# Kernel optimization log

Measured on AMD Instinct MI355X. Metric: run time of the kernel, lower is better.

The kernel has to match this reference:

```python
import jax, jax.numpy as jnp
import numpy as np

B, L, C = 1, 4096, 1024
H = 16
D = C // H  # head_dim = 64


def setup_inputs() -> dict:
    key = jax.random.key(0)
    k1, k2, k3 = jax.random.split(key, 3)
    scale_in = 1.0 / np.sqrt(C)
    return {
        "x": jax.random.normal(k1, (B, L, C), dtype=jnp.float32),
        "Wqkv": jax.random.normal(k2, (C, 3 * C), dtype=jnp.float32) * scale_in,
        "bqkv": jnp.zeros((3 * C,), dtype=jnp.float32),
        "Wout": jax.random.normal(k3, (C, C), dtype=jnp.float32) * scale_in,
        "bout": jnp.zeros((C,), dtype=jnp.float32),
    }


def reference(x, Wqkv, bqkv, Wout, bout):
    Bx, Lx, Cx = x.shape
    qkv = x @ Wqkv + bqkv                             # [B, L, 3C]
    qkv = qkv.reshape(Bx, Lx, 3, H, D)
    qkv = jnp.transpose(qkv, (2, 0, 3, 1, 4))         # [3, B, H, L, D]
    q, k, v = qkv[0], qkv[1], qkv[2]
    scores = jnp.einsum("bhqd,bhkd->bhqk", q, k) / jnp.sqrt(jnp.float32(D))
    # causal mask: strictly upper triangle -> -inf
    causal = jnp.triu(jnp.ones((Lx, Lx), dtype=bool), k=1)
    scores = jnp.where(causal, -jnp.inf, scores)
    attn = jax.nn.softmax(scores, axis=-1)            # [B, H, L, L]
    out = jnp.einsum("bhqk,bhkd->bhqd", attn, v)      # [B, H, L, D]
    out = jnp.transpose(out, (0, 2, 1, 3)).reshape(Bx, Lx, Cx)
    return out @ Wout + bout
```

## Files before the change

kernel.cpp:

```cpp
#include <hip/hip_runtime.h>
#include <hip/hip_bf16.h>

typedef unsigned short u16;
typedef __bf16 bf16x8 __attribute__((ext_vector_type(8)));
typedef float f32x4 __attribute__((ext_vector_type(4)));

#define L_SEQ 4096
#define CDIM  1024
#define NH    16
#define HD    64
#define N_QKV 3072
#define ATT_STRIDE 88

static __device__ __forceinline__ float bf2f(u16 u) {
    union { float f; unsigned int i; } v; v.i = ((unsigned int)u) << 16; return v.f;
}
static __device__ __forceinline__ u16 f2bf(float f) {
    union { float f; unsigned int i; } v; v.f = f;
    unsigned int u = v.i;
    return (u16)((u + 0x7fffu + ((u >> 16) & 1u)) >> 16);
}

static __device__ __forceinline__ f32x4 mfma16x16x32(bf16x8 a, bf16x8 b, f32x4 c) {
    return __builtin_amdgcn_mfma_f32_16x16x32_bf16(a, b, c, 0, 0, 0);
}

typedef const __attribute__((address_space(1))) unsigned int* gas_u32;
typedef __attribute__((address_space(3))) unsigned int* las_u32;
static __device__ __forceinline__ void gload_lds16(const u16* g, u16* l) {
    __builtin_amdgcn_global_load_lds((gas_u32)g, (las_u32)l, 16, 0, 0);
}

__global__ __launch_bounds__(256) void k_cast_x(const float* __restrict__ src,
                                                u16* __restrict__ dst, int n8) {
    int i = blockIdx.x * 256 + threadIdx.x;
    if (i >= n8) return;
    const float4* s = (const float4*)(src + (size_t)i * 8);
    float4 a = s[0], b = s[1];
    u16 o[8] = { f2bf(a.x), f2bf(a.y), f2bf(a.z), f2bf(a.w),
                 f2bf(b.x), f2bf(b.y), f2bf(b.z), f2bf(b.w) };
    *(uint4*)(dst + (size_t)i * 8) = *(uint4*)o;
}

__global__ __launch_bounds__(256) void k_transpose_cast(const float* __restrict__ src,
                                                        u16* __restrict__ dst,
                                                        int R, int C) {
    __shared__ u16 tile[32][33];
    int c0 = blockIdx.x * 32, r0 = blockIdx.y * 32;
    int tx = threadIdx.x & 31, ty = threadIdx.x >> 5;
#pragma unroll
    for (int i = 0; i < 32; i += 8)
        tile[ty + i][tx] = f2bf(src[(size_t)(r0 + ty + i) * C + c0 + tx]);
    __syncthreads();
#pragma unroll
    for (int i = 0; i < 32; i += 8)
        dst[(size_t)(c0 + ty + i) * R + r0 + tx] = tile[tx][ty + i];
}

__global__ __launch_bounds__(256) void k_transpose_v(const u16* __restrict__ qkv,
                                                     u16* __restrict__ vt) {
    __shared__ u16 tile[32][33];
    int k0 = blockIdx.x * 32, d0 = blockIdx.y * 32, h = blockIdx.z;
    int tx = threadIdx.x & 31, ty = threadIdx.x >> 5;
#pragma unroll
    for (int i = 0; i < 32; i += 8)
        tile[ty + i][tx] = qkv[(size_t)(k0 + ty + i) * N_QKV + 2 * CDIM + h * HD + d0 + tx];
    __syncthreads();
#pragma unroll
    for (int i = 0; i < 32; i += 8)
        vt[(size_t)(h * HD + d0 + ty + i) * L_SEQ + k0 + tx] = tile[tx][ty + i];
}

template <typename OutT>
__global__ __launch_bounds__(256) void k_gemm_bt(const u16* __restrict__ A,
                                                 const u16* __restrict__ Bt,
                                                 const float* __restrict__ bias,
                                                 OutT* __restrict__ Cmat,
                                                 int M, int N, int K) {
    __shared__ alignas(16) u16 As[128 * 32];
    __shared__ alignas(16) u16 Bs[128 * 32];
    int t = threadIdx.x;
    int n0 = blockIdx.x * 128, m0 = blockIdx.y * 128;
    int l = t & 63, w = t >> 6;
    int wm = (w >> 1) * 64, wn = (w & 1) * 64;
    int lr = l & 15, lq = l >> 4;

    const f32x4 vzero = {0.f, 0.f, 0.f, 0.f};
    f32x4 acc[4][4];
#pragma unroll
    for (int mi = 0; mi < 4; mi++)
#pragma unroll
        for (int ni = 0; ni < 4; ni++) acc[mi][ni] = vzero;

    int ar = t >> 2;
    int ac = (t & 3) * 8;
    const u16* Ag = A + (size_t)(m0 + ar) * K + ac;
    const u16* Bg = Bt + (size_t)(n0 + ar) * K + ac;
    u16* AsD0 = &As[t * 8];
    u16* AsD1 = &As[t * 8 + 64 * 32];
    u16* BsD0 = &Bs[t * 8];
    u16* BsD1 = &Bs[t * 8 + 64 * 32];

    for (int k0 = 0; k0 < K; k0 += 32) {
        gload_lds16(Ag + k0,                     AsD0);
        gload_lds16(Ag + (size_t)64 * K + k0,    AsD1);
        gload_lds16(Bg + k0,                     BsD0);
        gload_lds16(Bg + (size_t)64 * K + k0,    BsD1);
        __syncthreads();

        bf16x8 af[4], bfr[4];
#pragma unroll
        for (int mi = 0; mi < 4; mi++)
            af[mi] = *(const bf16x8*)&As[(wm + mi * 16 + lr) * 32 + lq * 8];
#pragma unroll
        for (int ni = 0; ni < 4; ni++)
            bfr[ni] = *(const bf16x8*)&Bs[(wn + ni * 16 + lr) * 32 + lq * 8];
#pragma unroll
        for (int mi = 0; mi < 4; mi++)
#pragma unroll
            for (int ni = 0; ni < 4; ni++)
                acc[mi][ni] = mfma16x16x32(af[mi], bfr[ni], acc[mi][ni]);
        __syncthreads();
    }

#pragma unroll
    for (int ni = 0; ni < 4; ni++) {
        int col = n0 + wn + ni * 16 + lr;
        float bv = bias[col];
#pragma unroll
        for (int mi = 0; mi < 4; mi++) {
            int row = m0 + wm + mi * 16 + lq * 4;
#pragma unroll
            for (int r = 0; r < 4; r++) {
                float v = acc[mi][ni][r] + bv;
                if constexpr (sizeof(OutT) == 2)
                    Cmat[(size_t)(row + r) * N + col] = f2bf(v);
                else
                    Cmat[(size_t)(row + r) * N + col] = v;
            }
        }
    }
}

__global__ __launch_bounds__(256) void k_attn(const u16* __restrict__ qkv,
                                              const u16* __restrict__ vt,
                                              u16* __restrict__ attn) {
    __shared__ alignas(16) u16 Ks[64 * ATT_STRIDE];
    __shared__ alignas(16) u16 Vs[64 * ATT_STRIDE];

    int t = threadIdx.x;
    int l = t & 63, w = t >> 6;
    int h = blockIdx.y;
    int lr = l & 15, lq = l >> 4;
    int row8 = t >> 3;
    int ch = (t & 7) * 8;
    int qloc = w * 16 + lr;

    const f32x4 vzero = {0.f, 0.f, 0.f, 0.f};
    const u16* Kbase = qkv + (size_t)row8 * N_QKV + CDIM + h * HD + ch;
    const u16* Vbase = vt + (size_t)(h * HD + row8) * L_SEQ + ch;

#pragma unroll
    for (int phase = 0; phase < 2; phase++) {
        int tile = phase ? (63 - blockIdx.x) : blockIdx.x;
        int q0 = tile * 64;
        int nkv = tile + 1;

        bf16x8 bq[2];
        {
            const u16* Qg = qkv + (size_t)(q0 + qloc) * N_QKV + h * HD + lq * 8;
            union { uint4 u; u16 hh[8]; } q0u, q1u;
            q0u.u = *(const uint4*)(Qg);
            q1u.u = *(const uint4*)(Qg + 32);
            union { bf16x8 v; u16 hh[8]; } f0, f1;
#pragma unroll
            for (int j = 0; j < 8; j++) {
                f0.hh[j] = f2bf(bf2f(q0u.hh[j]) * 0.125f);
                f1.hh[j] = f2bf(bf2f(q1u.hh[j]) * 0.125f);
            }
            bq[0] = f0.v; bq[1] = f1.v;
        }

        f32x4 o[4];
#pragma unroll
        for (int dt = 0; dt < 4; dt++) o[dt] = vzero;
        float m_i = -1e30f, l_i = 0.f;

        uint4 rk0, rk1, rv0, rv1;
        {
            const u16* Kg = Kbase;
            rk0 = *(const uint4*)Kg;
            rk1 = *(const uint4*)(Kg + (size_t)32 * N_QKV);
            const u16* Vg = Vbase;
            rv0 = *(const uint4*)Vg;
            rv1 = *(const uint4*)(Vg + (size_t)32 * L_SEQ);
        }

        for (int it = 0; it < nkv; ++it) {
            *(uint4*)&Ks[row8 * ATT_STRIDE + ch]        = rk0;
            *(uint4*)&Ks[(row8 + 32) * ATT_STRIDE + ch] = rk1;
            *(uint4*)&Vs[row8 * ATT_STRIDE + ch]        = rv0;
            *(uint4*)&Vs[(row8 + 32) * ATT_STRIDE + ch] = rv1;
            __syncthreads();

            if (it + 1 < nkv) {
                int k1 = (it + 1) * 64;
                const u16* Kg = Kbase + (size_t)k1 * N_QKV;
                rk0 = *(const uint4*)Kg;
                rk1 = *(const uint4*)(Kg + (size_t)32 * N_QKV);
                const u16* Vg = Vbase + k1;
                rv0 = *(const uint4*)Vg;
                rv1 = *(const uint4*)(Vg + (size_t)32 * L_SEQ);
            }

            f32x4 s[4];
#pragma unroll
            for (int nt = 0; nt < 4; nt++) s[nt] = vzero;
#pragma unroll
            for (int ks = 0; ks < 2; ks++)
#pragma unroll
                for (int nt = 0; nt < 4; nt++) {
                    bf16x8 ak = *(const bf16x8*)&Ks[(nt * 16 + lr) * ATT_STRIDE + ks * 32 + lq * 8];
                    s[nt] = mfma16x16x32(ak, bq[ks], s[nt]);
                }

            bool diag = ((it * 64) == q0);
            float tmax = -1e30f;
#pragma unroll
            for (int nt = 0; nt < 4; nt++)
#pragma unroll
                for (int r = 0; r < 4; r++) {
                    float v = s[nt][r];
                    if (diag && (nt * 16 + lq * 4 + r > qloc)) v = -1e30f;
                    s[nt][r] = v;
                    tmax = fmaxf(tmax, v);
                }
            tmax = fmaxf(tmax, __shfl_xor(tmax, 16));
            tmax = fmaxf(tmax, __shfl_xor(tmax, 32));

            float mnew = fmaxf(m_i, tmax);
            float alpha = __expf(m_i - mnew);
            float rsum = 0.f;
#pragma unroll
            for (int nt = 0; nt < 4; nt++)
#pragma unroll
                for (int r = 0; r < 4; r++) {
                    float e = __expf(s[nt][r] - mnew);
                    s[nt][r] = e;
                    rsum += e;
                }
            rsum += __shfl_xor(rsum, 16);
            rsum += __shfl_xor(rsum, 32);
            l_i = l_i * alpha + rsum;
            m_i = mnew;
#pragma unroll
            for (int dt = 0; dt < 4; dt++)
#pragma unroll
                for (int r = 0; r < 4; r++) o[dt][r] *= alpha;

#pragma unroll
            for (int a = 0; a < 2; a++) {
                union { bf16x8 v; u16 hh[8]; } bp;
#pragma unroll
                for (int r = 0; r < 4; r++) {
                    bp.hh[r]     = f2bf(s[2 * a][r]);
                    bp.hh[r + 4] = f2bf(s[2 * a + 1][r]);
                }
#pragma unroll
                for (int dt = 0; dt < 4; dt++) {
                    union { bf16x8 v; uint2 u2[2]; } av;
                    const u16* vrow = &Vs[(dt * 16 + lr) * ATT_STRIDE + a * 32 + lq * 4];
                    av.u2[0] = *(const uint2*)(vrow);
                    av.u2[1] = *(const uint2*)(vrow + 16);
                    o[dt] = mfma16x16x32(av.v, bp.v, o[dt]);
                }
            }
            __syncthreads();
        }

        float inv = 1.0f / l_i;
        int qg = q0 + qloc;
#pragma unroll
        for (int dt = 0; dt < 4; dt++) {
            union { u16 hh[4]; uint2 u2; } eo;
#pragma unroll
            for (int r = 0; r < 4; r++) eo.hh[r] = f2bf(o[dt][r] * inv);
            *(uint2*)&attn[(size_t)qg * CDIM + h * HD + dt * 16 + lq * 4] = eo.u2;
        }
    }
}

extern "C" void kernel_launch(void* const* d_in, const int* in_sizes, int n_in,
                              void* d_out, int out_size, void* d_ws, size_t ws_size,
                              hipStream_t stream) {
    const float* x    = (const float*)d_in[0];
    const float* Wqkv = (const float*)d_in[1];
    const float* bqkv = (const float*)d_in[2];
    const float* Wout = (const float*)d_in[3];
    const float* bout = (const float*)d_in[4];
    float* out = (float*)d_out;

    char* ws = (char*)d_ws;
    u16* qkv   = (u16*)(ws);
    u16* xb    = (u16*)(ws + 25165824);
    u16* attn  = xb;
    u16* vt    = (u16*)(ws + 33554432);
    u16* wqkvt = (u16*)(ws + 41943040);
    u16* woutt = (u16*)(ws + 48234496);

    k_cast_x<<<dim3(2048), 256, 0, stream>>>(x, xb, 524288);
    k_transpose_cast<<<dim3(96, 32), 256, 0, stream>>>(Wqkv, wqkvt, 1024, 3072);
    k_transpose_cast<<<dim3(32, 32), 256, 0, stream>>>(Wout, woutt, 1024, 1024);
    k_gemm_bt<u16><<<dim3(24, 32), 256, 0, stream>>>(xb, wqkvt, bqkv, qkv, 4096, 3072, 1024);
    k_transpose_v<<<dim3(128, 2, 16), 256, 0, stream>>>(qkv, vt);
    k_attn<<<dim3(32, 16), 256, 0, stream>>>(qkv, vt, attn);
    k_gemm_bt<float><<<dim3(8, 32), 256, 0, stream>>>(attn, woutt, bout, out, 4096, 1024, 1024);
}
```

Baseline: 246.6 us.

## Fuse x cast into QKV GEMM, widen attention KV tile, remap heads

The separate fp32-to-bf16 cast kernel for x is removed. The QKV GEMM now loads fp32 A from global memory, converts it in registers and stores it to LDS, which saves one launch and a round trip through memory but loses the async global-to-LDS path for A. The attention kernel now processes 128 keys per iteration instead of 64, using larger K/V LDS buffers with new strides, and masks only on the last tile. This halves the loop iterations and barriers but uses more registers and LDS and wastes some masked work. The attention grid is flattened, with a block-to-head mapping that groups heads, likely for cache locality.

```diff
diff --git a/kernel.cpp b/kernel.cpp
--- a/kernel.cpp
+++ b/kernel.cpp
@@ -10,7 +10,8 @@
 #define NH    16
 #define HD    64
 #define N_QKV 3072
-#define ATT_STRIDE 88
+#define KSTRIDE 88
+#define VSTRIDE 136
 
 static __device__ __forceinline__ float bf2f(u16 u) {
     union { float f; unsigned int i; } v; v.i = ((unsigned int)u) << 16; return v.f;
@@ -29,17 +30,6 @@
 typedef __attribute__((address_space(3))) unsigned int* las_u32;
 static __device__ __forceinline__ void gload_lds16(const u16* g, u16* l) {
     __builtin_amdgcn_global_load_lds((gas_u32)g, (las_u32)l, 16, 0, 0);
-}
-
-__global__ __launch_bounds__(256) void k_cast_x(const float* __restrict__ src,
-                                                u16* __restrict__ dst, int n8) {
-    int i = blockIdx.x * 256 + threadIdx.x;
-    if (i >= n8) return;
-    const float4* s = (const float4*)(src + (size_t)i * 8);
-    float4 a = s[0], b = s[1];
-    u16 o[8] = { f2bf(a.x), f2bf(a.y), f2bf(a.z), f2bf(a.w),
-                 f2bf(b.x), f2bf(b.y), f2bf(b.z), f2bf(b.w) };
-    *(uint4*)(dst + (size_t)i * 8) = *(uint4*)o;
 }
 
 __global__ __launch_bounds__(256) void k_transpose_cast(const float* __restrict__ src,
@@ -71,11 +61,82 @@
         vt[(size_t)(h * HD + d0 + ty + i) * L_SEQ + k0 + tx] = tile[tx][ty + i];
 }
 
-template <typename OutT>
+__global__ __launch_bounds__(256) void k_gemm_a32(const float* __restrict__ A,
+                                                  const u16* __restrict__ Bt,
+                                                  const float* __restrict__ bias,
+                                                  u16* __restrict__ Cmat,
+                                                  int M, int N, int K) {
+    __shared__ alignas(16) u16 As[128 * 32];
+    __shared__ alignas(16) u16 Bs[128 * 32];
+    int t = threadIdx.x;
+    int n0 = blockIdx.x * 128, m0 = blockIdx.y * 128;
+    int l = t & 63, w = t >> 6;
+    int wm = (w >> 1) * 64, wn = (w & 1) * 64;
+    int lr = l & 15, lq = l >> 4;
+
+    const f32x4 vzero = {0.f, 0.f, 0.f, 0.f};
+    f32x4 acc[4][4];
+#pragma unroll
+    for (int mi = 0; mi < 4; mi++)
+#pragma unroll
+        for (int ni = 0; ni < 4; ni++) acc[mi][ni] = vzero;
+
+    int ar = t >> 2;
+    int ac = (t & 3) * 8;
+    const float* Ag0 = A + (size_t)(m0 + ar) * K + ac;
+    const float* Ag1 = A + (size_t)(m0 + ar + 64) * K + ac;
+    const u16* Bg = Bt + (size_t)(n0 + ar) * K + ac;
+    u16* BsD0 = &Bs[t * 8];
+    u16* BsD1 = &Bs[t * 8 + 64 * 32];
+
+    for (int k0 = 0; k0 < K; k0 += 32) {
+        gload_lds16(Bg + k0,                  BsD0);
+        gload_lds16(Bg + (size_t)64 * K + k0, BsD1);
+        float4 a0 = *(const float4*)(Ag0 + k0);
+        float4 a1 = *(const float4*)(Ag0 + k0 + 4);
+        float4 a2 = *(const float4*)(Ag1 + k0);
+        float4 a3 = *(const float4*)(Ag1 + k0 + 4);
+        u16 o0[8] = { f2bf(a0.x), f2bf(a0.y), f2bf(a0.z), f2bf(a0.w),
+                      f2bf(a1.x), f2bf(a1.y), f2bf(a1.z), f2bf(a1.w) };
+        u16 o1[8] = { f2bf(a2.x), f2bf(a2.y), f2bf(a2.z), f2bf(a2.w),
+                      f2bf(a3.x), f2bf(a3.y), f2bf(a3.z), f2bf(a3.w) };
+        *(uint4*)&As[ar * 32 + ac]        = *(uint4*)o0;
+        *(uint4*)&As[(ar + 64) * 32 + ac] = *(uint4*)o1;
+        __syncthreads();
+
+        bf16x8 af[4], bfr[4];
+#pragma unroll
+        for (int mi = 0; mi < 4; mi++)
+            af[mi] = *(const bf16x8*)&As[(wm + mi * 16 + lr) * 32 + lq * 8];
+#pragma unroll
+        for (int ni = 0; ni < 4; ni++)
+            bfr[ni] = *(const bf16x8*)&Bs[(wn + ni * 16 + lr) * 32 + lq * 8];
+#pragma unroll
+        for (int mi = 0; mi < 4; mi++)
+#pragma unroll
+            for (int ni = 0; ni < 4; ni++)
+                acc[mi][ni] = mfma16x16x32(af[mi], bfr[ni], acc[mi][ni]);
+        __syncthreads();
+    }
+
+#pragma unroll
+    for (int ni = 0; ni < 4; ni++) {
+        int col = n0 + wn + ni * 16 + lr;
+        float bv = bias[col];
+#pragma unroll
+        for (int mi = 0; mi < 4; mi++) {
+            int row = m0 + wm + mi * 16 + lq * 4;
+#pragma unroll
+            for (int r = 0; r < 4; r++)
+                Cmat[(size_t)(row + r) * N + col] = f2bf(acc[mi][ni][r] + bv);
+        }
+    }
+}
+
 __global__ __launch_bounds__(256) void k_gemm_bt(const u16* __restrict__ A,
                                                  const u16* __restrict__ Bt,
                                                  const float* __restrict__ bias,
-                                                 OutT* __restrict__ Cmat,
+                                                 float* __restrict__ Cmat,
                                                  int M, int N, int K) {
     __shared__ alignas(16) u16 As[128 * 32];
     __shared__ alignas(16) u16 Bs[128 * 32];
@@ -102,10 +163,10 @@
     u16* BsD1 = &Bs[t * 8 + 64 * 32];
 
     for (int k0 = 0; k0 < K; k0 += 32) {
-        gload_lds16(Ag + k0,                     AsD0);
-        gload_lds16(Ag + (size_t)64 * K + k0,    AsD1);
-        gload_lds16(Bg + k0,                     BsD0);
-        gload_lds16(Bg + (size_t)64 * K + k0,    BsD1);
+        gload_lds16(Ag + k0,                  AsD0);
+        gload_lds16(Ag + (size_t)64 * K + k0, AsD1);
+        gload_lds16(Bg + k0,                  BsD0);
+        gload_lds16(Bg + (size_t)64 * K + k0, BsD1);
         __syncthreads();
 
         bf16x8 af[4], bfr[4];
@@ -131,13 +192,8 @@
         for (int mi = 0; mi < 4; mi++) {
             int row = m0 + wm + mi * 16 + lq * 4;
 #pragma unroll
-            for (int r = 0; r < 4; r++) {
-                float v = acc[mi][ni][r] + bv;
-                if constexpr (sizeof(OutT) == 2)
-                    Cmat[(size_t)(row + r) * N + col] = f2bf(v);
-                else
-                    Cmat[(size_t)(row + r) * N + col] = v;
-            }
+            for (int r = 0; r < 4; r++)
+                Cmat[(size_t)(row + r) * N + col] = acc[mi][ni][r] + bv;
         }
     }
 }
@@ -145,26 +201,32 @@
 __global__ __launch_bounds__(256) void k_attn(const u16* __restrict__ qkv,
                                               const u16* __restrict__ vt,
                                               u16* __restrict__ attn) {
-    __shared__ alignas(16) u16 Ks[64 * ATT_STRIDE];
-    __shared__ alignas(16) u16 Vs[64 * ATT_STRIDE];
+    __shared__ alignas(16) u16 Ks[128 * KSTRIDE];
+    __shared__ alignas(16) u16 Vs[64 * VSTRIDE];
 
     int t = threadIdx.x;
     int l = t & 63, w = t >> 6;
-    int h = blockIdx.y;
+    int id = blockIdx.x;
+    int kk = id >> 3;
+    int h = (id & 7) + 8 * (kk >> 5);
+    int pairx = kk & 31;
     int lr = l & 15, lq = l >> 4;
-    int row8 = t >> 3;
-    int ch = (t & 7) * 8;
     int qloc = w * 16 + lr;
 
+    int krow = t >> 3;
+    int kch = (t & 7) * 8;
+    int vd = t >> 4;
+    int vko = (t & 15) * 8;
+
     const f32x4 vzero = {0.f, 0.f, 0.f, 0.f};
-    const u16* Kbase = qkv + (size_t)row8 * N_QKV + CDIM + h * HD + ch;
-    const u16* Vbase = vt + (size_t)(h * HD + row8) * L_SEQ + ch;
+    const u16* Kbase = qkv + (size_t)krow * N_QKV + CDIM + h * HD + kch;
+    const u16* Vbase = vt + (size_t)(h * HD + vd) * L_SEQ + vko;
 
 #pragma unroll
     for (int phase = 0; phase < 2; phase++) {
-        int tile = phase ? (63 - blockIdx.x) : blockIdx.x;
+        int tile = phase ? (63 - pairx) : pairx;
         int q0 = tile * 64;
-        int nkv = tile + 1;
+        int nkv = (tile + 2) >> 1;
 
         bf16x8 bq[2];
         {
@@ -186,52 +248,50 @@
         for (int dt = 0; dt < 4; dt++) o[dt] = vzero;
         float m_i = -1e30f, l_i = 0.f;
 
-        uint4 rk0, rk1, rv0, rv1;
-        {
-            const u16* Kg = Kbase;
-            rk0 = *(const uint4*)Kg;
-            rk1 = *(const uint4*)(Kg + (size_t)32 * N_QKV);
-            const u16* Vg = Vbase;
-            rv0 = *(const uint4*)Vg;
-            rv1 = *(const uint4*)(Vg + (size_t)32 * L_SEQ);
+        uint4 rk[4], rv[4];
+#pragma unroll
+        for (int s2 = 0; s2 < 4; s2++) {
+            rk[s2] = *(const uint4*)(Kbase + (size_t)(32 * s2) * N_QKV);
+            rv[s2] = *(const uint4*)(Vbase + (size_t)(16 * s2) * L_SEQ);
         }
 
         for (int it = 0; it < nkv; ++it) {
-            *(uint4*)&Ks[row8 * ATT_STRIDE + ch]        = rk0;
-            *(uint4*)&Ks[(row8 + 32) * ATT_STRIDE + ch] = rk1;
-            *(uint4*)&Vs[row8 * ATT_STRIDE + ch]        = rv0;
-            *(uint4*)&Vs[(row8 + 32) * ATT_STRIDE + ch] = rv1;
+#pragma unroll
+            for (int s2 = 0; s2 < 4; s2++) {
+                *(uint4*)&Ks[(krow + 32 * s2) * KSTRIDE + kch] = rk[s2];
+                *(uint4*)&Vs[(vd + 16 * s2) * VSTRIDE + vko]   = rv[s2];
+            }
             __syncthreads();
 
             if (it + 1 < nkv) {
-                int k1 = (it + 1) * 64;
-                const u16* Kg = Kbase + (size_t)k1 * N_QKV;
-                rk0 = *(const uint4*)Kg;
-                rk1 = *(const uint4*)(Kg + (size_t)32 * N_QKV);
-                const u16* Vg = Vbase + k1;
-                rv0 = *(const uint4*)Vg;
-                rv1 = *(const uint4*)(Vg + (size_t)32 * L_SEQ);
+                int k1 = (it + 1) * 128;
+#pragma unroll
+                for (int s2 = 0; s2 < 4; s2++) {
+                    rk[s2] = *(const uint4*)(Kbase + (size_t)(k1 + 32 * s2) * N_QKV);
+                    rv[s2] = *(const uint4*)(Vbase + k1 + (size_t)(16 * s2) * L_SEQ);
+                }
             }
 
-            f32x4 s[4];
-#pragma unroll
-            for (int nt = 0; nt < 4; nt++) s[nt] = vzero;
+            f32x4 s[8];
+#pragma unroll
+            for (int nt = 0; nt < 8; nt++) s[nt] = vzero;
 #pragma unroll
             for (int ks = 0; ks < 2; ks++)
 #pragma unroll
-                for (int nt = 0; nt < 4; nt++) {
-                    bf16x8 ak = *(const bf16x8*)&Ks[(nt * 16 + lr) * ATT_STRIDE + ks * 32 + lq * 8];
+                for (int nt = 0; nt < 8; nt++) {
+                    bf16x8 ak = *(const bf16x8*)&Ks[(nt * 16 + lr) * KSTRIDE + ks * 32 + lq * 8];
                     s[nt] = mfma16x16x32(ak, bq[ks], s[nt]);
                 }
 
-            bool diag = ((it * 64) == q0);
+            bool last = (it == nkv - 1);
+            int k0 = it * 128;
             float tmax = -1e30f;
 #pragma unroll
-            for (int nt = 0; nt < 4; nt++)
+            for (int nt = 0; nt < 8; nt++)
 #pragma unroll
                 for (int r = 0; r < 4; r++) {
                     float v = s[nt][r];
-                    if (diag && (nt * 16 + lq * 4 + r > qloc)) v = -1e30f;
+                    if (last && (k0 + nt * 16 + lq * 4 + r > q0 + qloc)) v = -1e30f;
                     s[nt][r] = v;
                     tmax = fmaxf(tmax, v);
                 }
@@ -242,7 +302,7 @@
             float alpha = __expf(m_i - mnew);
             float rsum = 0.f;
 #pragma unroll
-            for (int nt = 0; nt < 4; nt++)
+            for (int nt = 0; nt < 8; nt++)
 #pragma unroll
                 for (int r = 0; r < 4; r++) {
                     float e = __expf(s[nt][r] - mnew);
@@ -259,7 +319,7 @@
                 for (int r = 0; r < 4; r++) o[dt][r] *= alpha;
 
 #pragma unroll
-            for (int a = 0; a < 2; a++) {
+            for (int a = 0; a < 4; a++) {
                 union { bf16x8 v; u16 hh[8]; } bp;
 #pragma unroll
                 for (int r = 0; r < 4; r++) {
@@ -269,7 +329,7 @@
 #pragma unroll
                 for (int dt = 0; dt < 4; dt++) {
                     union { bf16x8 v; uint2 u2[2]; } av;
-                    const u16* vrow = &Vs[(dt * 16 + lr) * ATT_STRIDE + a * 32 + lq * 4];
+                    const u16* vrow = &Vs[(dt * 16 + lr) * VSTRIDE + a * 32 + lq * 4];
                     av.u2[0] = *(const uint2*)(vrow);
                     av.u2[1] = *(const uint2*)(vrow + 16);
                     o[dt] = mfma16x16x32(av.v, bp.v, o[dt]);
@@ -302,17 +362,15 @@
 
     char* ws = (char*)d_ws;
     u16* qkv   = (u16*)(ws);
-    u16* xb    = (u16*)(ws + 25165824);
-    u16* attn  = xb;
+    u16* attn  = (u16*)(ws + 25165824);
     u16* vt    = (u16*)(ws + 33554432);
     u16* wqkvt = (u16*)(ws + 41943040);
     u16* woutt = (u16*)(ws + 48234496);
 
-    k_cast_x<<<dim3(2048), 256, 0, stream>>>(x, xb, 524288);
     k_transpose_cast<<<dim3(96, 32), 256, 0, stream>>>(Wqkv, wqkvt, 1024, 3072);
     k_transpose_cast<<<dim3(32, 32), 256, 0, stream>>>(Wout, woutt, 1024, 1024);
-    k_gemm_bt<u16><<<dim3(24, 32), 256, 0, stream>>>(xb, wqkvt, bqkv, qkv, 4096, 3072, 1024);
+    k_gemm_a32<<<dim3(24, 32), 256, 0, stream>>>(x, wqkvt, bqkv, qkv, 4096, 3072, 1024);
     k_transpose_v<<<dim3(128, 2, 16), 256, 0, stream>>>(qkv, vt);
-    k_attn<<<dim3(32, 16), 256, 0, stream>>>(qkv, vt, attn);
-    k_gemm_bt<float><<<dim3(8, 32), 256, 0, stream>>>(attn, woutt, bout, out, 4096, 1024, 1024);
-}
+    k_attn<<<dim3(512), 256, 0, stream>>>(qkv, vt, attn);
+    k_gemm_bt<<<dim3(8, 32), 256, 0, stream>>>(attn, woutt, bout, out, 4096, 1024, 1024);
+}
```

New measurement: 376.1 us. 52.5% more time.
